# Performance work log

Measured on AMD Instinct MI355X. Metric: run time of the kernel, lower is better.

Reference implementation:

```python
import jax, jax.numpy as jnp
import numpy as np

M = 12          # persons per frame
K = 2           # partition channels from conv1da (1024 = 2*512)
D = 512         # GCN channel dim / LSTM hidden
C_IN = 4096     # backbone feature dim
NUM_CLASSES = 8


def setup_inputs() -> dict:
    key = jax.random.key(0)
    ks = jax.random.split(key, 8)
    N, T = 16, 32
    NT = N * T
    base_out = jax.random.normal(ks[0], (NT, M, C_IN), dtype=jnp.float32)
    dist = jax.random.uniform(ks[1], (N, T, 3, K, M, M), dtype=jnp.float32)
    # conv1da: Conv1d(4096 -> 1024, k=1, bias=False) == matmul with [1024, 4096]
    w_a = jax.random.normal(ks[2], (K * D, C_IN), dtype=jnp.float32) * 0.02
    # LSTM(512, 512, 1): torch gate order i, f, g, o
    s = 1.0 / np.sqrt(D)
    w_ih = jax.random.uniform(ks[3], (4 * D, D), minval=-s, maxval=s, dtype=jnp.float32)
    w_hh = jax.random.uniform(ks[4], (4 * D, D), minval=-s, maxval=s, dtype=jnp.float32)
    b_ih = jax.random.uniform(ks[5], (4 * D,), minval=-s, maxval=s, dtype=jnp.float32)
    b_hh = jax.random.uniform(ks[6], (4 * D,), minval=-s, maxval=s, dtype=jnp.float32)
    # gclassifier: Linear(512 -> num_classes)
    w_cls = jax.random.normal(ks[7], (NUM_CLASSES, D), dtype=jnp.float32) * 0.01
    b_cls = jnp.zeros((NUM_CLASSES,), dtype=jnp.float32)
    return {"base_out": base_out, "dist": dist, "w_a": w_a,
            "w_ih": w_ih, "w_hh": w_hh, "b_ih": b_ih, "b_hh": b_hh,
            "w_cls": w_cls, "b_cls": b_cls, "n_videos": N}


def reference(base_out, dist, w_a, w_ih, w_hh, b_ih, b_hh, w_cls, b_cls, n_videos):
    NT = base_out.shape[0]
    N = n_videos
    T = NT // N
    # conv1da (1x1 conv, no bias): [NT, M, 4096] -> [NT, K*D, M] -> [NT, K, D, M]
    node1 = jnp.einsum('nmc,oc->nom', base_out, w_a).reshape(NT, K, D, M)
    # fused three-way adjacency aggregation: node1a + node1b + node1c
    A = (dist[:, :, 2] + dist[:, :, 1] + dist[:, :, 0]).reshape(NT, K, M, M)
    node = jnp.einsum('nkcv,nkvw->ncw', node1, A)  # [NT, D, M]
    node = jax.nn.relu(node)
    # AdaptiveAvgPool1d(1) over the M persons
    pooled = node.mean(axis=2)                      # [NT, D]
    seq = pooled.reshape(N, T, D)
    # torch nn.LSTM default batch_first=False: iterates over axis 0 (N), batch=T
    def step(carry, x_t):
        h, c = carry
        g = x_t @ w_ih.T + b_ih + h @ w_hh.T + b_hh  # [T, 4D]
        i, f, gg, o = jnp.split(g, 4, axis=-1)
        c = jax.nn.sigmoid(f) * c + jax.nn.sigmoid(i) * jnp.tanh(gg)
        h = jax.nn.sigmoid(o) * jnp.tanh(c)
        return (h, c), h
    h0 = jnp.zeros((T, D), dtype=seq.dtype)
    c0 = jnp.zeros((T, D), dtype=seq.dtype)
    _, hs = jax.lax.scan(step, (h0, c0), seq)       # [N, T, D]
    last = hs[:, -1, :]                              # video_feat[:, -1, :]
    return last @ w_cls.T + b_cls                    # [N, num_classes]
```

## Files before the change

### kernel.cpp

```cpp
#include <hip/hip_runtime.h>
#include <math.h>

#define MM 12
#define KK 2
#define DD 512
#define CIN 4096
#define NCLS 8
#define NV 16
#define TT 32

typedef unsigned long long u64;
typedef __attribute__((ext_vector_type(8))) __bf16 bf16x8;
typedef __attribute__((ext_vector_type(4))) float f32x4;

#define PART_F   0
#define POOLED_F 786432
#define TAGP_F   794624
#define TAGGX_F  794752
#define HGLOB_F  796800
#define GX_F     813184
#define PART_KS_STRIDE (192 * 1024)

#define MFMA_BF16(A, B, C) __builtin_amdgcn_mfma_f32_16x16x32_bf16((A), (B), (C), 0, 0, 0)
#define LOADR(p)      __hip_atomic_load((p), __ATOMIC_RELAXED, __HIP_MEMORY_SCOPE_AGENT)
#define LOADACQ(p)    __hip_atomic_load((p), __ATOMIC_ACQUIRE, __HIP_MEMORY_SCOPE_AGENT)
#define STOREREL(p, v) __hip_atomic_store((p), (v), __ATOMIC_RELEASE, __HIP_MEMORY_SCOPE_AGENT)
#define LOADS(p)      __hip_atomic_load((p), __ATOMIC_RELAXED, __HIP_MEMORY_SCOPE_SYSTEM)
#define EXCHS(p, v)   (void)__hip_atomic_exchange((p), (v), __ATOMIC_RELAXED, __HIP_MEMORY_SCOPE_SYSTEM)

static __device__ __forceinline__ u64 ld_sc0(const u64* p) {
  u64 v;
  asm volatile("global_load_dwordx2 %0, %1, off sc0\n\ts_waitcnt vmcnt(0)"
               : "=v"(v) : "v"(p) : "memory");
  return v;
}
static __device__ __forceinline__ void st_sc0(u64* p, u64 v) {
  asm volatile("global_store_dwordx2 %0, %1, off sc0" :: "v"(p), "v"(v) : "memory");
}

static __device__ __forceinline__ void cvt_store(
    unsigned short* __restrict__ hb, unsigned short* __restrict__ lb,
    int idx, float4 v) {
  unsigned ux = __float_as_uint(v.x), uy = __float_as_uint(v.y);
  unsigned uz = __float_as_uint(v.z), uw = __float_as_uint(v.w);
  *(uint2*)&hb[idx] = make_uint2((ux >> 16) | (uy & 0xFFFF0000u),
                                 (uz >> 16) | (uw & 0xFFFF0000u));
  unsigned lx = __float_as_uint(v.x - __uint_as_float(ux & 0xFFFF0000u));
  unsigned ly = __float_as_uint(v.y - __uint_as_float(uy & 0xFFFF0000u));
  unsigned lz = __float_as_uint(v.z - __uint_as_float(uz & 0xFFFF0000u));
  unsigned lw = __float_as_uint(v.w - __uint_as_float(uw & 0xFFFF0000u));
  *(uint2*)&lb[idx] = make_uint2((lx >> 16) | (ly & 0xFFFF0000u),
                                 (lz >> 16) | (lw & 0xFFFF0000u));
}

__global__ __launch_bounds__(64, 1) void k_gemm(
    const float* __restrict__ base_out, const float* __restrict__ w_a,
    float* __restrict__ part)
{
  const int wg = blockIdx.x;
  const int ks = wg & 3;
  const int ot = (wg >> 2) & 63;
  const int jq = (wg >> 8) & 3;
  const int cc0 = ks * 1024;
  const int lane = threadIdx.x;

  __shared__ __align__(16) unsigned short Ah[16 * 40], Al[16 * 40];
  __shared__ __align__(16) unsigned short Bh[48 * 40], Bl[48 * 40];

  const int sq = lane & 7;
  const int sr = lane >> 3;

  unsigned boff[6];
#pragma unroll
  for (int rep = 0; rep < 6; ++rep) {
    const int jl = sr + 8 * rep;
    const int j = jq * 48 + jl;
    const int n = j / 12, m = j - n * 12;
    boff[rep] = (unsigned)(((n * TT + 31) * MM + m) * CIN + cc0 + sq * 4);
  }
  unsigned aoff[2];
#pragma unroll
  for (int repA = 0; repA < 2; ++repA)
    aoff[repA] = (unsigned)((ot * 16 + sr + 8 * repA) * CIN + cc0 + sq * 4);

  f32x4 acc0 = {0.f, 0.f, 0.f, 0.f}, acc1 = acc0, acc2 = acc0;

  float4 pa[2], pb[6];
#pragma unroll
  for (int repA = 0; repA < 2; ++repA) pa[repA] = *(const float4*)&w_a[aoff[repA]];
#pragma unroll
  for (int rep = 0; rep < 6; ++rep) pb[rep] = *(const float4*)&base_out[boff[rep]];

  for (int st = 0; st < 32; ++st) {
#pragma unroll
    for (int repA = 0; repA < 2; ++repA)
      cvt_store(Ah, Al, (sr + 8 * repA) * 40 + sq * 4, pa[repA]);
#pragma unroll
    for (int rep = 0; rep < 6; ++rep)
      cvt_store(Bh, Bl, (sr + 8 * rep) * 40 + sq * 4, pb[rep]);
    if (st < 31) {
#pragma unroll
      for (int repA = 0; repA < 2; ++repA) {
        aoff[repA] += 32;
        pa[repA] = *(const float4*)&w_a[aoff[repA]];
      }
#pragma unroll
      for (int rep = 0; rep < 6; ++rep) {
        boff[rep] += 32;
        pb[rep] = *(const float4*)&base_out[boff[rep]];
      }
    }
    const int koff = (lane >> 4) * 8;
    const int fra = (lane & 15) * 40 + koff;
    bf16x8 oh = *(const bf16x8*)&Ah[fra];
    bf16x8 ol = *(const bf16x8*)&Al[fra];
    {
      const int r0 = (0 * 16 + (lane & 15)) * 40 + koff;
      bf16x8 jh = *(const bf16x8*)&Bh[r0], jl = *(const bf16x8*)&Bl[r0];
      acc0 = MFMA_BF16(jh, oh, acc0);
      acc0 = MFMA_BF16(jh, ol, acc0);
      acc0 = MFMA_BF16(jl, oh, acc0);
    }
    {
      const int r1 = (1 * 16 + (lane & 15)) * 40 + koff;
      bf16x8 jh = *(const bf16x8*)&Bh[r1], jl = *(const bf16x8*)&Bl[r1];
      acc1 = MFMA_BF16(jh, oh, acc1);
      acc1 = MFMA_BF16(jh, ol, acc1);
      acc1 = MFMA_BF16(jl, oh, acc1);
    }
    {
      const int r2 = (2 * 16 + (lane & 15)) * 40 + koff;
      bf16x8 jh = *(const bf16x8*)&Bh[r2], jl = *(const bf16x8*)&Bl[r2];
      acc2 = MFMA_BF16(jh, oh, acc2);
      acc2 = MFMA_BF16(jh, ol, acc2);
      acc2 = MFMA_BF16(jl, oh, acc2);
    }
  }
  const int o = ot * 16 + (lane & 15);
  const int jr = (lane >> 4) * 4;
#pragma unroll
  for (int r = 0; r < 4; ++r) {
    part[((size_t)ks * 192 + jq * 48 + 0 * 16 + jr + r) * 1024 + o] = acc0[r];
    part[((size_t)ks * 192 + jq * 48 + 1 * 16 + jr + r) * 1024 + o] = acc1[r];
    part[((size_t)ks * 192 + jq * 48 + 2 * 16 + jr + r) * 1024 + o] = acc2[r];
  }
}

__global__ __launch_bounds__(1024, 1) void k_rest(
    const float* __restrict__ dist, const float* __restrict__ part,
    float* __restrict__ pooled,
    const float* __restrict__ w_ih, const float* __restrict__ w_hh,
    const float* __restrict__ b_ih, const float* __restrict__ b_hh,
    const float* __restrict__ w_cls, const float* __restrict__ b_cls,
    unsigned* __restrict__ tagP, unsigned* __restrict__ tagGX,
    float* __restrict__ gxg, u64* __restrict__ hg64, float* __restrict__ out)
{
  const int wg = blockIdx.x;
  const int tid = threadIdx.x;

  __shared__ __align__(16) float whh_s[64][516];
  __shared__ float gx_s[16][64];
  __shared__ __align__(16) float h_s[DD];
  __shared__ float dot_s[64];
  __shared__ float Asum_s[2][KK * MM * MM];

  const int role = wg & 7;

  if (role == 5) {
    const int pq = wg >> 3;
    if (pq >= 8) return;
    for (int f = tid; f < 2 * KK * MM * MM; f += 1024) {
      const int nn = f / (KK * MM * MM), ff = f - nn * (KK * MM * MM);
      const unsigned dbase = (unsigned)(((2 * pq + nn) * TT + 31) * (3 * KK * MM * MM));
      Asum_s[nn][ff] = dist[dbase + ff] + dist[dbase + KK * MM * MM + ff]
                     + dist[dbase + 2 * KK * MM * MM + ff];
    }
    __syncthreads();
    {
      const int g = tid >> 5;
      const int pwg = pq * 32 + g;
      const int n = pwg >> 4, cb = (pwg & 15) * 32;
      const int c = cb + (tid & 31);
      float nd[KK][MM];
#pragma unroll
      for (int k = 0; k < KK; ++k)
#pragma unroll
        for (int v = 0; v < MM; ++v) {
          const size_t off = (size_t)(n * MM + v) * 1024 + k * DD + c;
          nd[k][v] = part[off] + part[off + PART_KS_STRIDE]
                   + part[off + 2 * PART_KS_STRIDE] + part[off + 3 * PART_KS_STRIDE];
        }
      float accm = 0.f;
#pragma unroll
      for (int w = 0; w < MM; ++w) {
        float sw = 0.f;
#pragma unroll
        for (int k = 0; k < KK; ++k)
#pragma unroll
          for (int v = 0; v < MM; ++v) sw += nd[k][v] * Asum_s[n - 2 * pq][(k * MM + v) * MM + w];
        accm += fmaxf(sw, 0.f);
      }
      pooled[n * DD + c] = accm * (1.f / 12.f);
    }
    __syncthreads();
    if (tid == 0) STOREREL(&tagP[pq * 16], 1u);
    return;
  }

  if (role != 0) {
    const int k = role;
    if (k > 4) return;
    const int m = wg >> 3;
    const int dd = m + 32 * (k - 1);
    if (tid < 64) {
      bool done;
      do {
        int t0 = (int)LOADR(&tagP[(tid & 7) * 16]);
        done = __all(t0 == 1);
      } while (!done);
    }
    __syncthreads();
    (void)LOADACQ(&tagP[0]);
    if (tid < 256) {
      const int n = tid & 15, j = tid >> 4;
      const int gr = dd * 16 + j;
      const float4* wr = (const float4*)&w_ih[(size_t)gr * DD];
      const float4* pv = (const float4*)&pooled[(size_t)n * DD];
      float a = 0.f;
#pragma unroll 8
      for (int q = 0; q < DD / 4; ++q) {
        float4 x = wr[q], y = pv[q];
        a += x.x * y.x + x.y * y.y + x.z * y.z + x.w * y.w;
      }
      gxg[m * 1024 + n * 64 + (k - 1) * 16 + j] = a + b_ih[gr] + b_hh[gr];
    }
    __syncthreads();
    if (tid == 0) STOREREL(&tagGX[dd * 16], 1u);
    return;
  }

  const int w = wg >> 3;

  for (int f = tid; f < 64 * 128; f += 1024) {
    const int rr = f >> 7, c4 = (f & 127) * 4;
    const int grow = (rr >> 4) * DD + w * 16 + (rr & 15);
    *(float4*)&whh_s[rr][c4] = *(const float4*)&w_hh[(size_t)grow * DD + c4];
  }
  if (tid < 64) {
    bool done;
    do {
      int t0 = (int)LOADR(&tagGX[(w + 32 * (tid & 3)) * 16]);
      done = __all(t0 == 1);
    } while (!done);
  }
  __syncthreads();
  gx_s[tid >> 6][tid & 63] =
      __uint_as_float(LOADS((const unsigned*)&gxg[w * 1024 + tid]));
  __syncthreads();

  {
    float c_reg = 0.f;
    const int r = tid >> 4;
    const int lj = tid & 15;

    for (int s = 0; s < NV; ++s) {
      if (s == 0) {
        if (tid < DD) h_s[tid] = 0.f;
      } else {
        if (tid < DD) {
          const u64* p = &hg64[(size_t)(s - 1) * DD + tid];
          u64 v = ld_sc0(p);
          while ((unsigned)v != (unsigned)s) {
            v = LOADS(p);
            if ((unsigned)v == (unsigned)s) break;
            v = ld_sc0(p);
          }
          h_s[tid] = __uint_as_float((unsigned)(v >> 32));
        }
      }
      __syncthreads();

      float p = 0.f;
      const float4* wrow = (const float4*)&whh_s[r][0];
      const float4* hv4 = (const float4*)h_s;
#pragma unroll
      for (int q = 0; q < 8; ++q) {
        float4 wv = wrow[lj + 16 * q];
        float4 hv = hv4[lj + 16 * q];
        p += wv.x * hv.x + wv.y * hv.y + wv.z * hv.z + wv.w * hv.w;
      }
#pragma unroll
      for (int off = 8; off; off >>= 1) p += __shfl_down(p, off, 16);
      if (lj == 0) dot_s[r] = p;
      __syncthreads();

      if (tid < 16) {
        const float pi = gx_s[s][tid]      + dot_s[tid];
        const float pf = gx_s[s][16 + tid] + dot_s[16 + tid];
        const float pg = gx_s[s][32 + tid] + dot_s[32 + tid];
        const float po = gx_s[s][48 + tid] + dot_s[48 + tid];
        const float si = 1.f / (1.f + expf(-pi));
        const float sf = 1.f / (1.f + expf(-pf));
        const float so = 1.f / (1.f + expf(-po));
        c_reg = sf * c_reg + si * tanhf(pg);
        const float hn = so * tanhf(c_reg);
        const u64 pk = ((u64)__float_as_uint(hn) << 32) | (u64)(unsigned)(s + 1);
        u64* pp = &hg64[(size_t)s * DD + w * 16 + tid];
        st_sc0(pp, pk);
        EXCHS(pp, pk);
      }
    }
  }

  if (wg == 0) {
    float* scratch = &whh_s[0][0];
    if (tid < DD) {
      u64 vv[NV];
#pragma unroll
      for (int n = 0; n < NV; ++n) vv[n] = LOADS(&hg64[(size_t)n * DD + tid]);
#pragma unroll
      for (int n = 0; n < NV; ++n) {
        u64 v = vv[n];
        while ((unsigned)v != (unsigned)(n + 1))
          v = LOADS(&hg64[(size_t)n * DD + tid]);
        scratch[n * 516 + tid] = __uint_as_float((unsigned)(v >> 32));
      }
    }
    __syncthreads();
    if (tid < NV * NCLS) {
      const int n = tid >> 3, cl = tid & 7;
      const float4* hv = (const float4*)&scratch[n * 516];
      const float4* wv = (const float4*)(w_cls + (size_t)cl * DD);
      float a = b_cls[cl];
#pragma unroll 8
      for (int q = 0; q < DD / 4; ++q) {
        float4 x = hv[q], y = wv[q];
        a += x.x * y.x + x.y * y.y + x.z * y.z + x.w * y.w;
      }
      out[tid] = a;
    }
  }
}

extern "C" void kernel_launch(void* const* d_in, const int* in_sizes, int n_in,
                              void* d_out, int out_size, void* d_ws, size_t ws_size,
                              hipStream_t stream) {
  const float* base_out = (const float*)d_in[0];
  const float* dist     = (const float*)d_in[1];
  const float* w_a      = (const float*)d_in[2];
  const float* w_ih     = (const float*)d_in[3];
  const float* w_hh     = (const float*)d_in[4];
  const float* b_ih     = (const float*)d_in[5];
  const float* b_hh     = (const float*)d_in[6];
  const float* w_cls    = (const float*)d_in[7];
  const float* b_cls    = (const float*)d_in[8];
  float* out = (float*)d_out;

  float* ws = (float*)d_ws;
  float* part   = ws + PART_F;
  float* pooled = ws + POOLED_F;
  unsigned* tagP  = (unsigned*)(ws + TAGP_F);
  unsigned* tagGX = (unsigned*)(ws + TAGGX_F);
  u64* hg64 = (u64*)(ws + HGLOB_F);
  float* gxg = ws + GX_F;

  k_gemm<<<dim3(1024), 64, 0, stream>>>(base_out, w_a, part);
  k_rest<<<dim3(256), 1024, 0, stream>>>(dist, part, pooled, w_ih, w_hh,
                                         b_ih, b_hh, w_cls, b_cls,
                                         tagP, tagGX, gxg, hg64, out);
}
```

Before: 299.0 us.

## Split pooling stage into separate kernel, drop tagP spin-wait handshake

Moves the graph-aggregation and pooling work out of the persistent k_rest kernel into its own k_pool launch of 256 small blocks. The gx workgroups no longer spin on tagP flags, because kernel ordering now guarantees that pooled is ready. This removes the flag polling and lets pooling spread across more CUs, at the cost of one extra kernel launch and a grid-wide boundary between the stages. Only 32 of the 256 threads per block do the pooling arithmetic.

```diff
diff --git a/kernel.cpp b/kernel.cpp
--- a/kernel.cpp
+++ b/kernel.cpp
@@ -15,7 +15,6 @@
 
 #define PART_F   0
 #define POOLED_F 786432
-#define TAGP_F   794624
 #define TAGGX_F  794752
 #define HGLOB_F  796800
 #define GX_F     813184
@@ -146,14 +145,53 @@
   }
 }
 
+__global__ __launch_bounds__(256, 1) void k_pool(
+    const float* __restrict__ dist, const float* __restrict__ part,
+    float* __restrict__ pooled)
+{
+  const int wg = blockIdx.x;
+  const int tid = threadIdx.x;
+
+  __shared__ float Asum_s[KK * MM * MM];
+
+  const int n = wg >> 4, cb = (wg & 15) * 32;
+  const unsigned dbase = (unsigned)((n * TT + 31) * (3 * KK * MM * MM));
+  for (int f = tid; f < KK * MM * MM; f += 256)
+    Asum_s[f] = dist[dbase + f] + dist[dbase + KK * MM * MM + f]
+              + dist[dbase + 2 * KK * MM * MM + f];
+  __syncthreads();
+  if (tid < 32) {
+    const int c = cb + tid;
+    float nd[KK][MM];
+#pragma unroll
+    for (int k = 0; k < KK; ++k)
+#pragma unroll
+      for (int v = 0; v < MM; ++v) {
+        const size_t off = (size_t)(n * MM + v) * 1024 + k * DD + c;
+        nd[k][v] = part[off] + part[off + PART_KS_STRIDE]
+                 + part[off + 2 * PART_KS_STRIDE] + part[off + 3 * PART_KS_STRIDE];
+      }
+    float accm = 0.f;
+#pragma unroll
+    for (int w = 0; w < MM; ++w) {
+      float sw = 0.f;
+#pragma unroll
+      for (int k = 0; k < KK; ++k)
+#pragma unroll
+        for (int v = 0; v < MM; ++v) sw += nd[k][v] * Asum_s[(k * MM + v) * MM + w];
+      accm += fmaxf(sw, 0.f);
+    }
+    pooled[n * DD + c] = accm * (1.f / 12.f);
+  }
+}
+
 __global__ __launch_bounds__(1024, 1) void k_rest(
-    const float* __restrict__ dist, const float* __restrict__ part,
-    float* __restrict__ pooled,
+    const float* __restrict__ pooled,
     const float* __restrict__ w_ih, const float* __restrict__ w_hh,
     const float* __restrict__ b_ih, const float* __restrict__ b_hh,
     const float* __restrict__ w_cls, const float* __restrict__ b_cls,
-    unsigned* __restrict__ tagP, unsigned* __restrict__ tagGX,
-    float* __restrict__ gxg, u64* __restrict__ hg64, float* __restrict__ out)
+    unsigned* __restrict__ tagGX, float* __restrict__ gxg,
+    u64* __restrict__ hg64, float* __restrict__ out)
 {
   const int wg = blockIdx.x;
   const int tid = threadIdx.x;
@@ -162,65 +200,12 @@
   __shared__ float gx_s[16][64];
   __shared__ __align__(16) float h_s[DD];
   __shared__ float dot_s[64];
-  __shared__ float Asum_s[2][KK * MM * MM];
-
-  const int role = wg & 7;
-
-  if (role == 5) {
-    const int pq = wg >> 3;
-    if (pq >= 8) return;
-    for (int f = tid; f < 2 * KK * MM * MM; f += 1024) {
-      const int nn = f / (KK * MM * MM), ff = f - nn * (KK * MM * MM);
-      const unsigned dbase = (unsigned)(((2 * pq + nn) * TT + 31) * (3 * KK * MM * MM));
-      Asum_s[nn][ff] = dist[dbase + ff] + dist[dbase + KK * MM * MM + ff]
-                     + dist[dbase + 2 * KK * MM * MM + ff];
-    }
-    __syncthreads();
-    {
-      const int g = tid >> 5;
-      const int pwg = pq * 32 + g;
-      const int n = pwg >> 4, cb = (pwg & 15) * 32;
-      const int c = cb + (tid & 31);
-      float nd[KK][MM];
-#pragma unroll
-      for (int k = 0; k < KK; ++k)
-#pragma unroll
-        for (int v = 0; v < MM; ++v) {
-          const size_t off = (size_t)(n * MM + v) * 1024 + k * DD + c;
-          nd[k][v] = part[off] + part[off + PART_KS_STRIDE]
-                   + part[off + 2 * PART_KS_STRIDE] + part[off + 3 * PART_KS_STRIDE];
-        }
-      float accm = 0.f;
-#pragma unroll
-      for (int w = 0; w < MM; ++w) {
-        float sw = 0.f;
-#pragma unroll
-        for (int k = 0; k < KK; ++k)
-#pragma unroll
-          for (int v = 0; v < MM; ++v) sw += nd[k][v] * Asum_s[n - 2 * pq][(k * MM + v) * MM + w];
-        accm += fmaxf(sw, 0.f);
-      }
-      pooled[n * DD + c] = accm * (1.f / 12.f);
-    }
-    __syncthreads();
-    if (tid == 0) STOREREL(&tagP[pq * 16], 1u);
-    return;
-  }
-
-  if (role != 0) {
-    const int k = role;
+
+  if ((wg & 7) != 0) {
+    const int k = wg & 7;
     if (k > 4) return;
     const int m = wg >> 3;
     const int dd = m + 32 * (k - 1);
-    if (tid < 64) {
-      bool done;
-      do {
-        int t0 = (int)LOADR(&tagP[(tid & 7) * 16]);
-        done = __all(t0 == 1);
-      } while (!done);
-    }
-    __syncthreads();
-    (void)LOADACQ(&tagP[0]);
     if (tid < 256) {
       const int n = tid & 15, j = tid >> 4;
       const int gr = dd * 16 + j;
@@ -359,13 +344,12 @@
   float* ws = (float*)d_ws;
   float* part   = ws + PART_F;
   float* pooled = ws + POOLED_F;
-  unsigned* tagP  = (unsigned*)(ws + TAGP_F);
   unsigned* tagGX = (unsigned*)(ws + TAGGX_F);
   u64* hg64 = (u64*)(ws + HGLOB_F);
   float* gxg = ws + GX_F;
 
   k_gemm<<<dim3(1024), 64, 0, stream>>>(base_out, w_a, part);
-  k_rest<<<dim3(256), 1024, 0, stream>>>(dist, part, pooled, w_ih, w_hh,
-                                         b_ih, b_hh, w_cls, b_cls,
-                                         tagP, tagGX, gxg, hg64, out);
-}
+  k_pool<<<dim3(256), 256, 0, stream>>>(dist, part, pooled);
+  k_rest<<<dim3(256), 1024, 0, stream>>>(pooled, w_ih, w_hh, b_ih, b_hh,
+                                         w_cls, b_cls, tagGX, gxg, hg64, out);
+}
```

Result: faster. 260.6 us (-12.8%).
